# Kernel tuning notes

Measured on AMD Instinct MI355X. Metric: run time of the kernel, lower is better.

The kernel has to match this reference:

```python
import jax, jax.numpy as jnp
import numpy as np

N_NODES = 100000
N_EDGES = 1600000
F_IN = 128
HEADS = 4
C_OUT = 32
NEG_SLOPE = 0.2


def setup_inputs() -> dict:
    key = jax.random.key(0)
    k1, k2, k3, k4, k5, k6 = jax.random.split(key, 6)
    x = jax.random.normal(k1, (N_NODES, F_IN), dtype=jnp.float32)
    edge_index = jax.random.randint(k2, (2, N_EDGES), 0, N_NODES, dtype=jnp.int64)
    # glorot-ish scales
    W = jax.random.normal(k3, (F_IN, HEADS * C_OUT), dtype=jnp.float32) * (1.0 / np.sqrt(F_IN))
    att_src = jax.random.normal(k4, (HEADS, C_OUT), dtype=jnp.float32) * (1.0 / np.sqrt(C_OUT))
    att_dst = jax.random.normal(k5, (HEADS, C_OUT), dtype=jnp.float32) * (1.0 / np.sqrt(C_OUT))
    bias = jnp.zeros((HEADS * C_OUT,), dtype=jnp.float32)
    return {"x": x, "edge_index": edge_index, "W": W,
            "att_src": att_src, "att_dst": att_dst, "bias": bias}


def _gat_forward(x, edge_index, W, att_src, att_dst, bias):
    N = x.shape[0]
    H, C = att_src.shape
    h = (x @ W).reshape(N, H, C)                      # [N,H,C]
    # PyG GATConv default: add self-loops
    loops = jnp.arange(N, dtype=edge_index.dtype)
    src = jnp.concatenate([edge_index[0], loops])     # [E+N]
    dst = jnp.concatenate([edge_index[1], loops])
    a_src = jnp.einsum("nhc,hc->nh", h, att_src)      # [N,H]
    a_dst = jnp.einsum("nhc,hc->nh", h, att_dst)
    e = jax.nn.leaky_relu(a_src[src] + a_dst[dst], NEG_SLOPE)  # [E+N,H]
    # segment softmax over destination node (every node has a self-loop)
    m = jax.ops.segment_max(e, dst, num_segments=N)
    e = jnp.exp(e - m[dst])
    s = jax.ops.segment_sum(e, dst, num_segments=N)
    alpha = e / (s[dst] + 1e-16)                      # [E+N,H]
    msg = h[src] * alpha[:, :, None]                  # [E+N,H,C]
    out = jax.ops.segment_sum(msg, dst, num_segments=N).reshape(N, H * C)
    return jnp.tanh(out + bias)


def reference(x, edge_index, W, att_src, att_dst, bias):
    return _gat_forward(x, edge_index, W, att_src, att_dst, bias)
```

## Files before the change

kernel.cpp:

```cpp
#include <hip/hip_runtime.h>
#include <math.h>

#define NN 100000
#define NE 1600000
#define F_IN 128
#define HEADS 4
#define HC 128
#define NEG_SLOPE 0.2f
#define NBKT 391
#define BCAP 5120
#define LDK 136
#define NSTRIP 6250

typedef __attribute__((ext_vector_type(8))) short bf16x8;
typedef __attribute__((ext_vector_type(4))) float f32x4;
typedef __attribute__((ext_vector_type(2))) float f32x2;

static __device__ __forceinline__ short f2bf_rne(float f) {
    unsigned u = __float_as_uint(f);
    unsigned r = (u + 0x7FFFu + ((u >> 16) & 1u)) >> 16;
    return (short)r;
}
static __device__ __forceinline__ float bf2f(short s) {
    return __uint_as_float(((unsigned)(unsigned short)s) << 16);
}
static __device__ __forceinline__ unsigned cvt_pk_bf16(float a, float b) {
    unsigned r;
    asm("v_cvt_pk_bf16_f32 %0, %1, %2" : "=v"(r) : "v"(a), "v"(b));
    return r;
}

static __device__ __forceinline__ void pk_fma(f32x2& d, f32x2 a, f32x2 b) {
    asm("v_pk_fma_f32 %0, %1, %2, %0 op_sel:[0,0,0] op_sel_hi:[1,1,1]"
        : "+v"(d) : "v"(a), "v"(b));
}
static __device__ __forceinline__ void pk_add(f32x2& d, f32x2 a) {
    asm("v_pk_add_f32 %0, %1, %0 op_sel:[0,0] op_sel_hi:[1,1]"
        : "+v"(d) : "v"(a));
}
static __device__ __forceinline__ f32x2 mkpair(float a, float b) {
    f32x2 r; r.x = a; r.y = b; return r;
}

__global__ __launch_bounds__(256) void prep_kernel(
        const float* __restrict__ W, short* __restrict__ wt_hi, short* __restrict__ wt_lo,
        const int* __restrict__ ei, int* __restrict__ flag) {
    if (blockIdx.x == 0 && threadIdx.x < 64) {
        int l = threadIdx.x;
        int v = ei[2 * l + 1];
        for (int off = 1; off < 64; off <<= 1) v |= __shfl_xor(v, off);
        if (l == 0) *flag = (v == 0) ? 1 : 0;
    }
    int i = blockIdx.x * 256 + threadIdx.x;
    if (i >= F_IN * HC) return;
    int k = i >> 7, n = i & 127;
    float f = W[k * HC + n];
    short hb = f2bf_rne(f);
    wt_hi[n * F_IN + k] = hb;
    wt_lo[n * F_IN + k] = f2bf_rne(f - bf2f(hb));
}

__global__ __launch_bounds__(256) void bucket_scatter_kernel(
        const int* __restrict__ ei, const int* __restrict__ flag,
        int* __restrict__ bcur, unsigned* __restrict__ pairs) {
    __shared__ int lhist[NBKT];
    __shared__ int gbase[NBKT];
    int t = threadIdx.x;
    for (int i = t; i < NBKT; i += 256) lhist[i] = 0;
    __syncthreads();
    int is64 = *flag;
    int base = blockIdx.x * 4096;

    unsigned wrd[16];
    int meta[16];
#pragma unroll
    for (int it = 0; it < 16; ++it) {
        int e = base + it * 256 + t;
        if (e < NE) {
            int src = is64 ? ei[2 * e] : ei[e];
            int dst = is64 ? ei[2 * NE + 2 * e] : ei[NE + e];
            int b = dst >> 8;
            int r = atomicAdd(&lhist[b], 1);
            wrd[it] = (unsigned)src | ((unsigned)(dst & 255) << 17);
            meta[it] = b | (r << 9);
        } else {
            meta[it] = -1;
        }
    }
    __syncthreads();
    for (int i = t; i < NBKT; i += 256)
        gbase[i] = lhist[i] ? atomicAdd(&bcur[i], lhist[i]) : 0;
    __syncthreads();
#pragma unroll
    for (int it = 0; it < 16; ++it) {
        if (meta[it] >= 0) {
            int b = meta[it] & 511;
            int r = meta[it] >> 9;
            pairs[(size_t)b * BCAP + gbase[b] + r] = wrd[it];
        }
    }
}

__global__ __launch_bounds__(512) void mfma_gemm_kernel(
        const float* __restrict__ x, const short* __restrict__ wt_hi,
        const short* __restrict__ wt_lo, const float* __restrict__ att_src,
        const float* __restrict__ att_dst, unsigned short* __restrict__ h_bf,
        float* __restrict__ a_src, float* __restrict__ a_dst) {
    __shared__ short lw_hi[64 * LDK];
    __shared__ short lw_lo[64 * LDK];
    int t = threadIdx.x;
    int blk = blockIdx.x;

    for (int c = t; c < 1024; c += 512) {
        int n = c >> 4;
        int kk = (c & 15) * 8;
        *(bf16x8*)(lw_hi + n * LDK + kk) = *(const bf16x8*)(wt_hi + n * F_IN + kk);
        *(bf16x8*)(lw_lo + n * LDK + kk) = *(const bf16x8*)(wt_lo + n * F_IN + kk);
    }
    __syncthreads();

    int strip = blk * 8 + (t >> 6);
    int valid = strip < NSTRIP;
    int sclamp = valid ? strip : NSTRIP - 1;
    int lane = t & 63;
    int l15 = lane & 15;
    int q = lane >> 4;

    f32x4 acc[8];
#pragma unroll
    for (int nt = 0; nt < 8; ++nt) acc[nt] = (f32x4){0.f, 0.f, 0.f, 0.f};

    union BU { bf16x8 v; unsigned u[4]; };
    BU ah[4], al[4];
    const float* xp = x + (size_t)(sclamp * 16 + l15) * F_IN + q * 8;

#pragma unroll
    for (int ki = 0; ki < 4; ++ki) {
        float4 v0 = *(const float4*)(xp + ki * 32);
        float4 v1 = *(const float4*)(xp + ki * 32 + 4);
        float vv[8] = {v0.x, v0.y, v0.z, v0.w, v1.x, v1.y, v1.z, v1.w};
#pragma unroll
        for (int j = 0; j < 4; ++j) {
            float f0 = vv[2 * j], f1 = vv[2 * j + 1];
            unsigned hp = cvt_pk_bf16(f0, f1);
            ah[ki].u[j] = hp;
            float r0 = f0 - __uint_as_float(hp << 16);
            float r1 = f1 - __uint_as_float(hp & 0xFFFF0000u);
            al[ki].u[j] = cvt_pk_bf16(r0, r1);
        }
        int koff = ki * 32 + q * 8;
#pragma unroll
        for (int nt = 0; nt < 4; ++nt) {
            int lidx = (nt * 16 + l15) * LDK + koff;
            bf16x8 b_hi = *(const bf16x8*)(lw_hi + lidx);
            bf16x8 b_lo = *(const bf16x8*)(lw_lo + lidx);
            acc[nt] = __builtin_amdgcn_mfma_f32_16x16x32_bf16(ah[ki].v, b_hi, acc[nt], 0, 0, 0);
            acc[nt] = __builtin_amdgcn_mfma_f32_16x16x32_bf16(al[ki].v, b_hi, acc[nt], 0, 0, 0);
            acc[nt] = __builtin_amdgcn_mfma_f32_16x16x32_bf16(ah[ki].v, b_lo, acc[nt], 0, 0, 0);
        }
    }

    __syncthreads();
    for (int c = t; c < 1024; c += 512) {
        int n = c >> 4;
        int kk = (c & 15) * 8;
        *(bf16x8*)(lw_hi + n * LDK + kk) = *(const bf16x8*)(wt_hi + (64 + n) * F_IN + kk);
        *(bf16x8*)(lw_lo + n * LDK + kk) = *(const bf16x8*)(wt_lo + (64 + n) * F_IN + kk);
    }
    __syncthreads();

#pragma unroll
    for (int ki = 0; ki < 4; ++ki) {
        int koff = ki * 32 + q * 8;
#pragma unroll
        for (int nt = 0; nt < 4; ++nt) {
            int lidx = (nt * 16 + l15) * LDK + koff;
            bf16x8 b_hi = *(const bf16x8*)(lw_hi + lidx);
            bf16x8 b_lo = *(const bf16x8*)(lw_lo + lidx);
            acc[4 + nt] = __builtin_amdgcn_mfma_f32_16x16x32_bf16(ah[ki].v, b_hi, acc[4 + nt], 0, 0, 0);
            acc[4 + nt] = __builtin_amdgcn_mfma_f32_16x16x32_bf16(al[ki].v, b_hi, acc[4 + nt], 0, 0, 0);
            acc[4 + nt] = __builtin_amdgcn_mfma_f32_16x16x32_bf16(ah[ki].v, b_lo, acc[4 + nt], 0, 0, 0);
        }
    }

    if (!valid) return;

    int orow = strip * 16 + q * 4;
#pragma unroll
    for (int nt = 0; nt < 8; ++nt)
#pragma unroll
        for (int r = 0; r < 4; ++r)
            h_bf[(size_t)(orow + r) * HC + nt * 16 + l15] =
                (unsigned short)f2bf_rne(acc[nt][r]);

#pragma unroll
    for (int hd = 0; hd < 4; ++hd) {
        float as0 = att_src[hd * 32 + l15];
        float as1 = att_src[hd * 32 + 16 + l15];
        float ad0 = att_dst[hd * 32 + l15];
        float ad1 = att_dst[hd * 32 + 16 + l15];
#pragma unroll
        for (int r = 0; r < 4; ++r) {
            float ps = acc[2 * hd][r] * as0 + acc[2 * hd + 1][r] * as1;
            float pd = acc[2 * hd][r] * ad0 + acc[2 * hd + 1][r] * ad1;
#pragma unroll
            for (int off = 1; off < 16; off <<= 1) {
                ps += __shfl_xor(ps, off);
                pd += __shfl_xor(pd, off);
            }
            if (l15 == 0) {
                int row = orow + r;
                a_src[row * 4 + hd] = ps;
                a_dst[row * 4 + hd] = pd;
            }
        }
    }
}

__global__ __launch_bounds__(1024) void bucket_csr_kernel(
        const int* __restrict__ bcur, const unsigned* __restrict__ pairs,
        const float* __restrict__ a_src, const float* __restrict__ a_dst,
        int* __restrict__ deg, int* __restrict__ offsets,
        int* __restrict__ csr_src, unsigned* __restrict__ wal) {
    __shared__ unsigned lpairs[BCAP];
    __shared__ int sd[1024];
    __shared__ int cnt256[256];
    __shared__ int lcur[256];

    int b = blockIdx.x;
    int t = threadIdx.x;

    int partial = 0;
    for (int i = t; i < b; i += 1024) partial += bcur[i];
    sd[t] = partial;
    __syncthreads();
    for (int off = 512; off > 0; off >>= 1) {
        if (t < off) sd[t] += sd[t + off];
        __syncthreads();
    }
    int bktbase = sd[0];
    __syncthreads();

    if (t < 256) cnt256[t] = 0;
    __syncthreads();

    int cnt = bcur[b];
    const unsigned* __restrict__ bp = pairs + (size_t)b * BCAP;
    for (int i = t; i < cnt; i += 1024) {
        unsigned w = bp[i];
        lpairs[i] = w;
        atomicAdd(&cnt256[w >> 17], 1);
    }
    __syncthreads();

    if (t < 256) sd[t] = cnt256[t];
    __syncthreads();
    for (int off = 1; off < 256; off <<= 1) {
        int u = 0;
        if (t < 256 && t >= off) u = sd[t - off];
        __syncthreads();
        if (t < 256) sd[t] += u;
        __syncthreads();
    }
    if (t < 256) {
        int v = cnt256[t];
        int myoff = bktbase + sd[t] - v;
        int node = (b << 8) + t;
        if (node < NN) {
            deg[node] = v;
            offsets[node] = myoff;
        }
        lcur[t] = myoff;
    }
    __syncthreads();

    for (int i = t; i < cnt; i += 1024) {
        unsigned w = lpairs[i];
        int src = (int)(w & 0x1FFFFu);
        int dl = (int)(w >> 17);
        float4 as = ((const float4*)a_src)[src];
        float4 ad = ((const float4*)a_dst)[(b << 8) + dl];
        float e0 = as.x + ad.x; e0 = (e0 < 0.f) ? NEG_SLOPE * e0 : e0;
        float e1 = as.y + ad.y; e1 = (e1 < 0.f) ? NEG_SLOPE * e1 : e1;
        float e2 = as.z + ad.z; e2 = (e2 < 0.f) ? NEG_SLOPE * e2 : e2;
        float e3 = as.w + ad.w; e3 = (e3 < 0.f) ? NEG_SLOPE * e3 : e3;
        float w0 = __expf(e0), w1 = __expf(e1), w2 = __expf(e2), w3 = __expf(e3);
        int pos = atomicAdd(&lcur[dl], 1);
        csr_src[pos] = src;
        unsigned lo = (unsigned)(unsigned short)f2bf_rne(w0) |
                      ((unsigned)(unsigned short)f2bf_rne(w1) << 16);
        unsigned hi = (unsigned)(unsigned short)f2bf_rne(w2) |
                      ((unsigned)(unsigned short)f2bf_rne(w3) << 16);
        ((uint2*)wal)[pos] = make_uint2(lo, hi);
    }
}

__global__ __launch_bounds__(256) void gat_aggr_kernel(
        const int* __restrict__ offsets, const int* __restrict__ deg,
        const int* __restrict__ csr_src, const unsigned* __restrict__ wal,
        const float* __restrict__ a_src, const float* __restrict__ a_dst,
        const unsigned* __restrict__ h2, const float* __restrict__ bias,
        float* __restrict__ out) {
    int wid = (blockIdx.x * 256 + threadIdx.x) >> 6;
    int dst = __builtin_amdgcn_readfirstlane(wid);
    if (dst >= NN) return;
    int lane = threadIdx.x & 63;
    int hd = lane >> 4;
    unsigned hsel2 = (unsigned)(hd & 2);
    unsigned shamt = (hd & 1) ? 0u : 16u;

    int start = offsets[dst];
    int n = deg[dst];

    f32x2 accx2 = {0.f, 0.f}, accy2 = {0.f, 0.f}, ws2 = {0.f, 0.f};

    int j = 0;
    for (; j + 7 < n; j += 8) {
        int base = start + j;
        int s0 = csr_src[base + 0];
        int s1 = csr_src[base + 1];
        int s2 = csr_src[base + 2];
        int s3 = csr_src[base + 3];
        int s4 = csr_src[base + 4];
        int s5 = csr_src[base + 5];
        int s6 = csr_src[base + 6];
        int s7 = csr_src[base + 7];
        uint2 wv0 = ((const uint2*)wal)[base + 0];
        uint2 wv1 = ((const uint2*)wal)[base + 1];
        uint2 wv2 = ((const uint2*)wal)[base + 2];
        uint2 wv3 = ((const uint2*)wal)[base + 3];
        uint2 wv4 = ((const uint2*)wal)[base + 4];
        uint2 wv5 = ((const uint2*)wal)[base + 5];
        uint2 wv6 = ((const uint2*)wal)[base + 6];
        uint2 wv7 = ((const uint2*)wal)[base + 7];
        unsigned u0 = h2[(size_t)s0 * 64 + lane];
        unsigned u1 = h2[(size_t)s1 * 64 + lane];
        unsigned u2 = h2[(size_t)s2 * 64 + lane];
        unsigned u3 = h2[(size_t)s3 * 64 + lane];
        unsigned u4 = h2[(size_t)s4 * 64 + lane];
        unsigned u5 = h2[(size_t)s5 * 64 + lane];
        unsigned u6 = h2[(size_t)s6 * 64 + lane];
        unsigned u7 = h2[(size_t)s7 * 64 + lane];
#define EDGEPAIR(ua, ub, wva, wvb)                                              \
        {                                                                       \
            unsigned wsa = hsel2 ? wva.y : wva.x;                               \
            unsigned wsb = hsel2 ? wvb.y : wvb.x;                               \
            f32x2 wp = mkpair(__uint_as_float((wsa << shamt) & 0xFFFF0000u),    \
                              __uint_as_float((wsb << shamt) & 0xFFFF0000u));   \
            f32x2 hx = mkpair(__uint_as_float(ua << 16),                        \
                              __uint_as_float(ub << 16));                       \
            f32x2 hy = mkpair(__uint_as_float(ua & 0xFFFF0000u),                \
                              __uint_as_float(ub & 0xFFFF0000u));               \
            pk_add(ws2, wp);                                                    \
            pk_fma(accx2, wp, hx);                                              \
            pk_fma(accy2, wp, hy);                                              \
        }
        EDGEPAIR(u0, u1, wv0, wv1)
        EDGEPAIR(u2, u3, wv2, wv3)
        EDGEPAIR(u4, u5, wv4, wv5)
        EDGEPAIR(u6, u7, wv6, wv7)
    }
    for (; j + 1 < n; j += 2) {
        int base = start + j;
        int s0 = csr_src[base + 0];
        int s1 = csr_src[base + 1];
        uint2 wv0 = ((const uint2*)wal)[base + 0];
        uint2 wv1 = ((const uint2*)wal)[base + 1];
        unsigned u0 = h2[(size_t)s0 * 64 + lane];
        unsigned u1 = h2[(size_t)s1 * 64 + lane];
        EDGEPAIR(u0, u1, wv0, wv1)
    }
#undef EDGEPAIR
    float accx = accx2.x + accx2.y;
    float accy = accy2.x + accy2.y;
    float wsum = ws2.x + ws2.y;
    if (j < n) {
        int base = start + j;
        int s0 = csr_src[base];
        uint2 wv0 = ((const uint2*)wal)[base];
        unsigned u0 = h2[(size_t)s0 * 64 + lane];
        unsigned ws0 = hsel2 ? wv0.y : wv0.x;
        float w0 = __uint_as_float((ws0 << shamt) & 0xFFFF0000u);
        wsum += w0;
        accx += w0 * __uint_as_float(u0 << 16);
        accy += w0 * __uint_as_float(u0 & 0xFFFF0000u);
    }

    float e = a_src[dst * 4 + hd] + a_dst[dst * 4 + hd];
    e = (e < 0.f) ? NEG_SLOPE * e : e;
    float sf = __expf(e);
    float inv = 1.f / (wsum + sf + 1e-16f);

    unsigned us = h2[(size_t)dst * 64 + lane];
    float2 b2 = ((const float2*)bias)[lane];
    float ox = tanhf((accx + sf * __uint_as_float(us << 16)) * inv + b2.x);
    float oy = tanhf((accy + sf * __uint_as_float(us & 0xFFFF0000u)) * inv + b2.y);
    ((float2*)out)[(size_t)dst * 64 + lane] = make_float2(ox, oy);
}

extern "C" void kernel_launch(void* const* d_in, const int* in_sizes, int n_in,
                              void* d_out, int out_size, void* d_ws, size_t ws_size,
                              hipStream_t stream) {
    const float* x       = (const float*)d_in[0];
    const int*   ei      = (const int*)  d_in[1];
    const float* W       = (const float*)d_in[2];
    const float* att_src = (const float*)d_in[3];
    const float* att_dst = (const float*)d_in[4];
    const float* bias    = (const float*)d_in[5];
    float* out = (float*)d_out;

    unsigned short* h_bf = (unsigned short*)d_ws;
    float* a_src = (float*)(h_bf + (size_t)NN * HC);
    float* a_dst = a_src + (size_t)NN * HEADS;
    short* wt_hi = (short*)(a_dst + (size_t)NN * HEADS);
    short* wt_lo = wt_hi + F_IN * HC;
    int* flag    = (int*)(wt_lo + F_IN * HC);
    int* bcur    = flag + 4;
    int* deg     = bcur + NBKT + 1;
    int* offsets = deg + NN;
    int* csr_src = offsets + NN;
    unsigned* wal = (unsigned*)(csr_src + NE);
    unsigned* pairs = (unsigned*)(wal + (size_t)NE * 2);

    hipMemsetAsync(bcur, 0, NBKT * sizeof(int), stream);

    hipLaunchKernelGGL(prep_kernel, dim3(64), dim3(256), 0, stream,
                       W, wt_hi, wt_lo, ei, flag);

    hipLaunchKernelGGL(bucket_scatter_kernel, dim3((NE + 4095) / 4096), dim3(256), 0, stream,
                       ei, flag, bcur, pairs);

    hipLaunchKernelGGL(mfma_gemm_kernel, dim3(782), dim3(512), 0, stream,
                       x, wt_hi, wt_lo, att_src, att_dst, h_bf, a_src, a_dst);

    hipLaunchKernelGGL(bucket_csr_kernel, dim3(NBKT), dim3(1024), 0, stream,
                       bcur, pairs, a_src, a_dst, deg, offsets, csr_src, wal);

    hipLaunchKernelGGL(gat_aggr_kernel, dim3(NN * 64 / 256), dim3(256), 0, stream,
                       offsets, deg, csr_src, wal, a_src, a_dst,
                       (const unsigned*)h_bf, bias, out);
}
```

Before: 253.1 us.

## Drop W low-part split, split out attention dot kernel, vectorize edge loads

Several independent changes. The GEMM drops the W residual (wt_lo) term, going from 3 to 2 MFMAs per tile and loading all 128 columns of W into LDS at once, which lowers precision of h. The attention-coefficient dot products move out of the GEMM into a separate kernel that reads the bf16 h, adding a launch and an extra pass over h. The int64 edge path now reads int4 vectors, and the CSR build kernel issues up to four edges' gathers before processing them to raise memory-level parallelism.

```diff
diff --git a/kernel.cpp b/kernel.cpp
--- a/kernel.cpp
+++ b/kernel.cpp
@@ -43,7 +43,7 @@
 }
 
 __global__ __launch_bounds__(256) void prep_kernel(
-        const float* __restrict__ W, short* __restrict__ wt_hi, short* __restrict__ wt_lo,
+        const float* __restrict__ W, short* __restrict__ wt_hi,
         const int* __restrict__ ei, int* __restrict__ flag) {
     if (blockIdx.x == 0 && threadIdx.x < 64) {
         int l = threadIdx.x;
@@ -54,10 +54,7 @@
     int i = blockIdx.x * 256 + threadIdx.x;
     if (i >= F_IN * HC) return;
     int k = i >> 7, n = i & 127;
-    float f = W[k * HC + n];
-    short hb = f2bf_rne(f);
-    wt_hi[n * F_IN + k] = hb;
-    wt_lo[n * F_IN + k] = f2bf_rne(f - bf2f(hb));
+    wt_hi[n * F_IN + k] = f2bf_rne(W[k * HC + n]);
 }
 
 __global__ __launch_bounds__(256) void bucket_scatter_kernel(
@@ -73,18 +70,40 @@
 
     unsigned wrd[16];
     int meta[16];
-#pragma unroll
-    for (int it = 0; it < 16; ++it) {
-        int e = base + it * 256 + t;
-        if (e < NE) {
-            int src = is64 ? ei[2 * e] : ei[e];
-            int dst = is64 ? ei[2 * NE + 2 * e] : ei[NE + e];
-            int b = dst >> 8;
-            int r = atomicAdd(&lhist[b], 1);
-            wrd[it] = (unsigned)src | ((unsigned)(dst & 255) << 17);
-            meta[it] = b | (r << 9);
-        } else {
-            meta[it] = -1;
+    if (is64) {
+#pragma unroll
+        for (int it = 0; it < 8; ++it) {
+            int e = base + it * 512 + 2 * t;
+            if (e < NE) {
+                int4 sv = *(const int4*)(ei + 2 * (size_t)e);
+                int4 dv = *(const int4*)(ei + 2 * (size_t)NE + 2 * (size_t)e);
+                int b0 = dv.x >> 8;
+                int r0 = atomicAdd(&lhist[b0], 1);
+                wrd[2 * it] = (unsigned)sv.x | ((unsigned)(dv.x & 255) << 17);
+                meta[2 * it] = b0 | (r0 << 9);
+                int b1 = dv.z >> 8;
+                int r1 = atomicAdd(&lhist[b1], 1);
+                wrd[2 * it + 1] = (unsigned)sv.z | ((unsigned)(dv.z & 255) << 17);
+                meta[2 * it + 1] = b1 | (r1 << 9);
+            } else {
+                meta[2 * it] = -1;
+                meta[2 * it + 1] = -1;
+            }
+        }
+    } else {
+#pragma unroll
+        for (int it = 0; it < 16; ++it) {
+            int e = base + it * 256 + t;
+            if (e < NE) {
+                int src = ei[e];
+                int dst = ei[NE + e];
+                int b = dst >> 8;
+                int r = atomicAdd(&lhist[b], 1);
+                wrd[it] = (unsigned)src | ((unsigned)(dst & 255) << 17);
+                meta[it] = b | (r << 9);
+            } else {
+                meta[it] = -1;
+            }
         }
     }
     __syncthreads();
@@ -103,25 +122,19 @@
 
 __global__ __launch_bounds__(512) void mfma_gemm_kernel(
         const float* __restrict__ x, const short* __restrict__ wt_hi,
-        const short* __restrict__ wt_lo, const float* __restrict__ att_src,
-        const float* __restrict__ att_dst, unsigned short* __restrict__ h_bf,
-        float* __restrict__ a_src, float* __restrict__ a_dst) {
-    __shared__ short lw_hi[64 * LDK];
-    __shared__ short lw_lo[64 * LDK];
+        unsigned short* __restrict__ h_bf) {
+    __shared__ short lw[128 * LDK];
     int t = threadIdx.x;
-    int blk = blockIdx.x;
-
-    for (int c = t; c < 1024; c += 512) {
+
+    for (int c = t; c < 2048; c += 512) {
         int n = c >> 4;
         int kk = (c & 15) * 8;
-        *(bf16x8*)(lw_hi + n * LDK + kk) = *(const bf16x8*)(wt_hi + n * F_IN + kk);
-        *(bf16x8*)(lw_lo + n * LDK + kk) = *(const bf16x8*)(wt_lo + n * F_IN + kk);
-    }
-    __syncthreads();
-
-    int strip = blk * 8 + (t >> 6);
-    int valid = strip < NSTRIP;
-    int sclamp = valid ? strip : NSTRIP - 1;
+        *(bf16x8*)(lw + n * LDK + kk) = *(const bf16x8*)(wt_hi + n * F_IN + kk);
+    }
+    __syncthreads();
+
+    int strip = blockIdx.x * 8 + (t >> 6);
+    if (strip >= NSTRIP) return;
     int lane = t & 63;
     int l15 = lane & 15;
     int q = lane >> 4;
@@ -131,59 +144,31 @@
     for (int nt = 0; nt < 8; ++nt) acc[nt] = (f32x4){0.f, 0.f, 0.f, 0.f};
 
     union BU { bf16x8 v; unsigned u[4]; };
-    BU ah[4], al[4];
-    const float* xp = x + (size_t)(sclamp * 16 + l15) * F_IN + q * 8;
+    const float* xp = x + (size_t)(strip * 16 + l15) * F_IN + q * 8;
 
 #pragma unroll
     for (int ki = 0; ki < 4; ++ki) {
         float4 v0 = *(const float4*)(xp + ki * 32);
         float4 v1 = *(const float4*)(xp + ki * 32 + 4);
         float vv[8] = {v0.x, v0.y, v0.z, v0.w, v1.x, v1.y, v1.z, v1.w};
+        BU ah, al;
 #pragma unroll
         for (int j = 0; j < 4; ++j) {
             float f0 = vv[2 * j], f1 = vv[2 * j + 1];
             unsigned hp = cvt_pk_bf16(f0, f1);
-            ah[ki].u[j] = hp;
+            ah.u[j] = hp;
             float r0 = f0 - __uint_as_float(hp << 16);
             float r1 = f1 - __uint_as_float(hp & 0xFFFF0000u);
-            al[ki].u[j] = cvt_pk_bf16(r0, r1);
+            al.u[j] = cvt_pk_bf16(r0, r1);
         }
         int koff = ki * 32 + q * 8;
 #pragma unroll
-        for (int nt = 0; nt < 4; ++nt) {
-            int lidx = (nt * 16 + l15) * LDK + koff;
-            bf16x8 b_hi = *(const bf16x8*)(lw_hi + lidx);
-            bf16x8 b_lo = *(const bf16x8*)(lw_lo + lidx);
-            acc[nt] = __builtin_amdgcn_mfma_f32_16x16x32_bf16(ah[ki].v, b_hi, acc[nt], 0, 0, 0);
-            acc[nt] = __builtin_amdgcn_mfma_f32_16x16x32_bf16(al[ki].v, b_hi, acc[nt], 0, 0, 0);
-            acc[nt] = __builtin_amdgcn_mfma_f32_16x16x32_bf16(ah[ki].v, b_lo, acc[nt], 0, 0, 0);
-        }
-    }
-
-    __syncthreads();
-    for (int c = t; c < 1024; c += 512) {
-        int n = c >> 4;
-        int kk = (c & 15) * 8;
-        *(bf16x8*)(lw_hi + n * LDK + kk) = *(const bf16x8*)(wt_hi + (64 + n) * F_IN + kk);
-        *(bf16x8*)(lw_lo + n * LDK + kk) = *(const bf16x8*)(wt_lo + (64 + n) * F_IN + kk);
-    }
-    __syncthreads();
-
-#pragma unroll
-    for (int ki = 0; ki < 4; ++ki) {
-        int koff = ki * 32 + q * 8;
-#pragma unroll
-        for (int nt = 0; nt < 4; ++nt) {
-            int lidx = (nt * 16 + l15) * LDK + koff;
-            bf16x8 b_hi = *(const bf16x8*)(lw_hi + lidx);
-            bf16x8 b_lo = *(const bf16x8*)(lw_lo + lidx);
-            acc[4 + nt] = __builtin_amdgcn_mfma_f32_16x16x32_bf16(ah[ki].v, b_hi, acc[4 + nt], 0, 0, 0);
-            acc[4 + nt] = __builtin_amdgcn_mfma_f32_16x16x32_bf16(al[ki].v, b_hi, acc[4 + nt], 0, 0, 0);
-            acc[4 + nt] = __builtin_amdgcn_mfma_f32_16x16x32_bf16(ah[ki].v, b_lo, acc[4 + nt], 0, 0, 0);
-        }
-    }
-
-    if (!valid) return;
+        for (int nt = 0; nt < 8; ++nt) {
+            bf16x8 bh = *(const bf16x8*)(lw + (nt * 16 + l15) * LDK + koff);
+            acc[nt] = __builtin_amdgcn_mfma_f32_16x16x32_bf16(ah.v, bh, acc[nt], 0, 0, 0);
+            acc[nt] = __builtin_amdgcn_mfma_f32_16x16x32_bf16(al.v, bh, acc[nt], 0, 0, 0);
+        }
+    }
 
     int orow = strip * 16 + q * 4;
 #pragma unroll
@@ -192,28 +177,34 @@
         for (int r = 0; r < 4; ++r)
             h_bf[(size_t)(orow + r) * HC + nt * 16 + l15] =
                 (unsigned short)f2bf_rne(acc[nt][r]);
-
-#pragma unroll
-    for (int hd = 0; hd < 4; ++hd) {
-        float as0 = att_src[hd * 32 + l15];
-        float as1 = att_src[hd * 32 + 16 + l15];
-        float ad0 = att_dst[hd * 32 + l15];
-        float ad1 = att_dst[hd * 32 + 16 + l15];
-#pragma unroll
-        for (int r = 0; r < 4; ++r) {
-            float ps = acc[2 * hd][r] * as0 + acc[2 * hd + 1][r] * as1;
-            float pd = acc[2 * hd][r] * ad0 + acc[2 * hd + 1][r] * ad1;
-#pragma unroll
-            for (int off = 1; off < 16; off <<= 1) {
-                ps += __shfl_xor(ps, off);
-                pd += __shfl_xor(pd, off);
-            }
-            if (l15 == 0) {
-                int row = orow + r;
-                a_src[row * 4 + hd] = ps;
-                a_dst[row * 4 + hd] = pd;
-            }
-        }
+}
+
+__global__ __launch_bounds__(256) void attdot_kernel(
+        const unsigned* __restrict__ h2, const float* __restrict__ att_src,
+        const float* __restrict__ att_dst,
+        float* __restrict__ a_src, float* __restrict__ a_dst) {
+    int row = (blockIdx.x * 256 + threadIdx.x) >> 6;
+    if (row >= NN) return;
+    int lane = threadIdx.x & 63;
+    int hd = lane >> 4;
+    int l15 = lane & 15;
+    unsigned u = h2[(size_t)row * 64 + lane];
+    float f0 = __uint_as_float(u << 16);
+    float f1 = __uint_as_float(u & 0xFFFF0000u);
+    float as0 = att_src[hd * 32 + 2 * l15];
+    float as1 = att_src[hd * 32 + 2 * l15 + 1];
+    float ad0 = att_dst[hd * 32 + 2 * l15];
+    float ad1 = att_dst[hd * 32 + 2 * l15 + 1];
+    float ps = f0 * as0 + f1 * as1;
+    float pd = f0 * ad0 + f1 * ad1;
+#pragma unroll
+    for (int off = 1; off < 16; off <<= 1) {
+        ps += __shfl_xor(ps, off);
+        pd += __shfl_xor(pd, off);
+    }
+    if (l15 == 0) {
+        a_src[row * 4 + hd] = ps;
+        a_dst[row * 4 + hd] = pd;
     }
 }
 
@@ -274,25 +265,49 @@
     }
     __syncthreads();
 
-    for (int i = t; i < cnt; i += 1024) {
-        unsigned w = lpairs[i];
-        int src = (int)(w & 0x1FFFFu);
-        int dl = (int)(w >> 17);
-        float4 as = ((const float4*)a_src)[src];
-        float4 ad = ((const float4*)a_dst)[(b << 8) + dl];
-        float e0 = as.x + ad.x; e0 = (e0 < 0.f) ? NEG_SLOPE * e0 : e0;
-        float e1 = as.y + ad.y; e1 = (e1 < 0.f) ? NEG_SLOPE * e1 : e1;
-        float e2 = as.z + ad.z; e2 = (e2 < 0.f) ? NEG_SLOPE * e2 : e2;
-        float e3 = as.w + ad.w; e3 = (e3 < 0.f) ? NEG_SLOPE * e3 : e3;
-        float w0 = __expf(e0), w1 = __expf(e1), w2 = __expf(e2), w3 = __expf(e3);
-        int pos = atomicAdd(&lcur[dl], 1);
-        csr_src[pos] = src;
-        unsigned lo = (unsigned)(unsigned short)f2bf_rne(w0) |
-                      ((unsigned)(unsigned short)f2bf_rne(w1) << 16);
-        unsigned hi = (unsigned)(unsigned short)f2bf_rne(w2) |
-                      ((unsigned)(unsigned short)f2bf_rne(w3) << 16);
-        ((uint2*)wal)[pos] = make_uint2(lo, hi);
-    }
+#define CSR_EMIT(w_, as_, ad_)                                                  \
+    {                                                                           \
+        int src_ = (int)(w_ & 0x1FFFFu);                                        \
+        int dl_ = (int)(w_ >> 17);                                              \
+        float e0 = as_.x + ad_.x; e0 = (e0 < 0.f) ? NEG_SLOPE * e0 : e0;        \
+        float e1 = as_.y + ad_.y; e1 = (e1 < 0.f) ? NEG_SLOPE * e1 : e1;        \
+        float e2 = as_.z + ad_.z; e2 = (e2 < 0.f) ? NEG_SLOPE * e2 : e2;        \
+        float e3 = as_.w + ad_.w; e3 = (e3 < 0.f) ? NEG_SLOPE * e3 : e3;        \
+        float w0 = __expf(e0), w1 = __expf(e1), w2 = __expf(e2), w3 = __expf(e3); \
+        int pos = atomicAdd(&lcur[dl_], 1);                                     \
+        csr_src[pos] = src_;                                                    \
+        unsigned lo = (unsigned)(unsigned short)f2bf_rne(w0) |                  \
+                      ((unsigned)(unsigned short)f2bf_rne(w1) << 16);           \
+        unsigned hi = (unsigned)(unsigned short)f2bf_rne(w2) |                  \
+                      ((unsigned)(unsigned short)f2bf_rne(w3) << 16);           \
+        ((uint2*)wal)[pos] = make_uint2(lo, hi);                                \
+    }
+
+    {
+        int i1 = t + 1024, i2 = t + 2048, i3 = t + 3072;
+        int v0 = (t < cnt), v1 = (i1 < cnt), v2 = (i2 < cnt), v3 = (i3 < cnt);
+        unsigned w0 = 0, w1 = 0, w2 = 0, w3 = 0;
+        if (v0) w0 = lpairs[t];
+        if (v1) w1 = lpairs[i1];
+        if (v2) w2 = lpairs[i2];
+        if (v3) w3 = lpairs[i3];
+        float4 as0, ad0, as1, ad1, as2, ad2, as3, ad3;
+        if (v0) { as0 = ((const float4*)a_src)[w0 & 0x1FFFFu]; ad0 = ((const float4*)a_dst)[(b << 8) + (w0 >> 17)]; }
+        if (v1) { as1 = ((const float4*)a_src)[w1 & 0x1FFFFu]; ad1 = ((const float4*)a_dst)[(b << 8) + (w1 >> 17)]; }
+        if (v2) { as2 = ((const float4*)a_src)[w2 & 0x1FFFFu]; ad2 = ((const float4*)a_dst)[(b << 8) + (w2 >> 17)]; }
+        if (v3) { as3 = ((const float4*)a_src)[w3 & 0x1FFFFu]; ad3 = ((const float4*)a_dst)[(b << 8) + (w3 >> 17)]; }
+        if (v0) CSR_EMIT(w0, as0, ad0);
+        if (v1) CSR_EMIT(w1, as1, ad1);
+        if (v2) CSR_EMIT(w2, as2, ad2);
+        if (v3) CSR_EMIT(w3, as3, ad3);
+        for (int i = t + 4096; i < cnt; i += 1024) {
+            unsigned w = lpairs[i];
+            float4 as = ((const float4*)a_src)[w & 0x1FFFFu];
+            float4 ad = ((const float4*)a_dst)[(b << 8) + (w >> 17)];
+            CSR_EMIT(w, as, ad);
+        }
+    }
+#undef CSR_EMIT
 }
 
 __global__ __launch_bounds__(256) void gat_aggr_kernel(
@@ -413,8 +428,7 @@
     float* a_src = (float*)(h_bf + (size_t)NN * HC);
     float* a_dst = a_src + (size_t)NN * HEADS;
     short* wt_hi = (short*)(a_dst + (size_t)NN * HEADS);
-    short* wt_lo = wt_hi + F_IN * HC;
-    int* flag    = (int*)(wt_lo + F_IN * HC);
+    int* flag    = (int*)(wt_hi + F_IN * HC);
     int* bcur    = flag + 4;
     int* deg     = bcur + NBKT + 1;
     int* offsets = deg + NN;
@@ -425,13 +439,16 @@
     hipMemsetAsync(bcur, 0, NBKT * sizeof(int), stream);
 
     hipLaunchKernelGGL(prep_kernel, dim3(64), dim3(256), 0, stream,
-                       W, wt_hi, wt_lo, ei, flag);
+                       W, wt_hi, ei, flag);
 
     hipLaunchKernelGGL(bucket_scatter_kernel, dim3((NE + 4095) / 4096), dim3(256), 0, stream,
                        ei, flag, bcur, pairs);
 
     hipLaunchKernelGGL(mfma_gemm_kernel, dim3(782), dim3(512), 0, stream,
-                       x, wt_hi, wt_lo, att_src, att_dst, h_bf, a_src, a_dst);
+                       x, wt_hi, h_bf);
+
+    hipLaunchKernelGGL(attdot_kernel, dim3(NN * 64 / 256), dim3(256), 0, stream,
+                       (const unsigned*)h_bf, att_src, att_dst, a_src, a_dst);
 
     hipLaunchKernelGGL(bucket_csr_kernel, dim3(NBKT), dim3(1024), 0, stream,
                        bcur, pairs, a_src, a_dst, deg, offsets, csr_src, wal);
```

Result: no change. 254.0 us (+0.3%).
